# Optimization experiments

Measured on AMD Instinct MI355X. Metric: run time of the kernel, lower is better.

Reference implementation:

```python
import jax, jax.numpy as jnp
import numpy as np

N, E = 50000, 800000
IN_DIM, OUT_DIM, H = 256, 128, 8
GEO_HID = 16  # RBF feature dim and geo_mlp hidden dim


def setup_inputs() -> dict:
    key = jax.random.key(0)
    ks = jax.random.split(key, 16)
    def lin(k, fan_out, fan_in):
        kw, kb = jax.random.split(k)
        lim = 1.0 / np.sqrt(fan_in)
        W = jax.random.uniform(kw, (fan_out, fan_in), jnp.float32, -lim, lim)
        b = jax.random.uniform(kb, (fan_out,), jnp.float32, -lim, lim)
        return W, b
    Wq, bq = lin(ks[0], OUT_DIM, IN_DIM)
    Wk, bk = lin(ks[1], OUT_DIM, IN_DIM)
    Wv, bv = lin(ks[2], OUT_DIM, IN_DIM)
    Wo, bo = lin(ks[3], OUT_DIM, OUT_DIM)
    Wg1, bg1 = lin(ks[4], GEO_HID, GEO_HID)
    Wg2, bg2 = lin(ks[5], H, GEO_HID)
    x = jax.random.normal(ks[6], (N, IN_DIM), jnp.float32)
    edge_index = jax.random.randint(ks[7], (2, E), 0, N, jnp.int64)
    edge_dist = jax.random.uniform(ks[8], (E,), jnp.float32) * 6.0
    return {"x": x, "edge_index": edge_index, "edge_dist": edge_dist,
            "Wq": Wq, "bq": bq, "Wk": Wk, "bk": bk, "Wv": Wv, "bv": bv,
            "Wo": Wo, "bo": bo, "Wg1": Wg1, "bg1": bg1, "Wg2": Wg2, "bg2": bg2}


def reference(x, edge_index, edge_dist, Wq, bq, Wk, bk, Wv, bv, Wo, bo, Wg1, bg1, Wg2, bg2):
    n = x.shape[0]
    num_heads = Wg2.shape[0]
    head_dim = Wq.shape[0] // num_heads
    scale = 1.0 / (head_dim ** 0.5)

    q = (x @ Wq.T + bq).reshape(n, num_heads, head_dim)
    k = (x @ Wk.T + bk).reshape(n, num_heads, head_dim)
    v = (x @ Wv.T + bv).reshape(n, num_heads, head_dim)

    # RBF expansion: 16 centers in [0, 6], gamma = 1.0
    centers = jnp.linspace(0.0, 6.0, GEO_HID)
    rbf = jnp.exp(-(edge_dist[:, None] - centers) ** 2)          # [E, 16]
    geo_bias = jax.nn.relu(rbf @ Wg1.T + bg1) @ Wg2.T + bg2      # [E, H]

    row, col = edge_index[0], edge_index[1]
    attn = (q[row] * k[col]).sum(-1) * scale + geo_bias          # [E, H]

    # segment softmax over incoming edges per destination node (row)
    m = jax.ops.segment_max(attn, row, num_segments=n)           # [N, H]
    e = jnp.exp(attn - m[row])
    s = jax.ops.segment_sum(e, row, num_segments=n)              # [N, H]
    a = e / (s[row] + 1e-12)                                     # [E, H]

    out = jax.ops.segment_sum(v[col] * a[:, :, None], row, num_segments=n)
    out = out.reshape(n, num_heads * head_dim)
    return out @ Wo.T + bo
```

## Files before the change

### kernel.cpp

```cpp
#include <hip/hip_runtime.h>
#include <math.h>

#define IN_DIM 256
#define OUT_DIM 128
#define NH 8
#define HD 16
#define GH 16
#define TBL 1024
#define LOG2E 1.44269504f
#define RCAP 64
#define BINSH 6
#define BCAP 1408

typedef __attribute__((ext_vector_type(8))) short short8;
typedef __attribute__((ext_vector_type(4))) float floatx4;

__device__ __forceinline__ unsigned short f2bf(float f) {
    union { float f; unsigned u; } v; v.f = f;
    unsigned r = v.u + 0x7fffu + ((v.u >> 16) & 1u);
    return (unsigned short)(r >> 16);
}
__device__ __forceinline__ float bf2f(unsigned short h) {
    union { unsigned u; float f; } v; v.u = ((unsigned)h) << 16;
    return v.f;
}
__device__ __forceinline__ void split1(float f, unsigned short& h, unsigned short& l) {
    h = f2bf(f);
    l = f2bf(f - bf2f(h));
}
__device__ __forceinline__ float bflo(unsigned u) { return __uint_as_float(u << 16); }
__device__ __forceinline__ float bfhi(unsigned u) { return __uint_as_float(u & 0xffff0000u); }

__global__ __launch_bounds__(256) void prep_all_kernel(
    const float* __restrict__ Wq, const float* __restrict__ Wk,
    const float* __restrict__ Wv, const float* __restrict__ Wo,
    unsigned short* __restrict__ wh, unsigned short* __restrict__ wl,
    unsigned short* __restrict__ wo_h, unsigned short* __restrict__ wo_l,
    const float* __restrict__ Wg1, const float* __restrict__ bg1,
    const float* __restrict__ Wg2, const float* __restrict__ bg2,
    float* __restrict__ tbl, int* __restrict__ gbin,
    int nbins, int nwm, int nwo, int ngeo) {
    int bx = blockIdx.x;
    int t = threadIdx.x;

    if (bx < 3 * nwm) {
        int m = bx / nwm;
        int i = (bx - m * nwm) * 256 + t;
        if (i >= (OUT_DIM * IN_DIM) / 4) return;
        const float* W = (m == 0) ? Wq : (m == 1) ? Wk : Wv;
        float4 f = ((const float4*)W)[i];
        ushort4 h, l;
        split1(f.x, h.x, l.x); split1(f.y, h.y, l.y);
        split1(f.z, h.z, l.z); split1(f.w, h.w, l.w);
        size_t base = (size_t)m * (OUT_DIM * IN_DIM) / 4;
        ((ushort4*)wh)[base + i] = h;
        ((ushort4*)wl)[base + i] = l;
        return;
    }
    bx -= 3 * nwm;
    if (bx < nwo) {
        int i = bx * 256 + t;
        if (i >= (OUT_DIM * OUT_DIM) / 4) return;
        float4 f = ((const float4*)Wo)[i];
        ushort4 h, l;
        split1(f.x, h.x, l.x); split1(f.y, h.y, l.y);
        split1(f.z, h.z, l.z); split1(f.w, h.w, l.w);
        ((ushort4*)wo_h)[i] = h;
        ((ushort4*)wo_l)[i] = l;
        return;
    }
    bx -= nwo;
    if (bx < ngeo) {
        int i = bx * 256 + t;
        if (i >= TBL) return;
        float d = (float)i * (6.0f / (float)(TBL - 1));
        float rbf[GH];
#pragma unroll
        for (int j = 0; j < GH; ++j) {
            float c = 0.4f * (float)j;
            float tt = d - c;
            rbf[j] = __expf(-tt * tt);
        }
        float hid[GH];
#pragma unroll
        for (int j = 0; j < GH; ++j) {
            float acc = bg1[j];
#pragma unroll
            for (int kk = 0; kk < GH; ++kk) acc += rbf[kk] * Wg1[j * GH + kk];
            hid[j] = fmaxf(acc, 0.0f);
        }
#pragma unroll
        for (int h = 0; h < NH; ++h) {
            float acc = bg2[h];
#pragma unroll
            for (int j = 0; j < GH; ++j) acc += hid[j] * Wg2[h * GH + j];
            tbl[i * NH + h] = acc * LOG2E;
        }
        return;
    }
    for (int i = t; i < nbins; i += 256) gbin[i] = 0;
}

__global__ __launch_bounds__(512, 4) void qkv_kernel(
    const float* __restrict__ x,
    const unsigned short* __restrict__ wh, const unsigned short* __restrict__ wl,
    const float* __restrict__ bq, const float* __restrict__ bk, const float* __restrict__ bv,
    float* __restrict__ q, unsigned short* __restrict__ kb, unsigned short* __restrict__ vb,
    const int* __restrict__ ei, const float* __restrict__ edist,
    int* __restrict__ gbin, int2* __restrict__ binbuf,
    int Nn, int E_, int nxb, int nb1, int nbins) {
    __shared__ unsigned short xh_s[128 * 40];
    __shared__ unsigned short xl_s[128 * 40];
    __shared__ unsigned short wh_s[128 * 40];
    __shared__ unsigned short wl_s[128 * 40];

    const int tid = threadIdx.x;
    int bx = blockIdx.x;

    if (bx < nb1) {
        int* hist = (int*)xh_s;
        const int e0 = bx * 4096;
        for (int b = tid; b < nbins; b += 512) hist[b] = 0;
        __syncthreads();
#pragma unroll
        for (int i = 0; i < 8; ++i) {
            int e = e0 + tid + i * 512;
            if (e < E_) atomicAdd(&hist[ei[e] >> BINSH], 1);
        }
        __syncthreads();
        for (int b = tid; b < nbins; b += 512) {
            int h = hist[b];
            int base = 0;
            if (h) base = atomicAdd(&gbin[b], h);
            hist[b] = base;
        }
        __syncthreads();
#pragma unroll
        for (int i = 0; i < 8; ++i) {
            int e = e0 + tid + i * 512;
            if (e < E_) {
                int row = ei[e];
                int bin = row >> BINSH;
                int r = atomicAdd(&hist[bin], 1);
                float u = edist[e] * ((float)(TBL - 1) / 6.0f);
                u = fminf(fmaxf(u, 0.0f), (float)(TBL - 1));
                if (r < BCAP)
                    binbuf[(size_t)bin * BCAP + r] =
                        make_int2((ei[E_ + e] & 0x1FFFF) | ((row & 63) << 17), __float_as_int(u));
            }
        }
        return;
    }
    bx -= nb1;

    const int wsel = bx / nxb;
    const int n0 = (bx - wsel * nxb) * 128;
    const unsigned short* W_h = wh + (size_t)wsel * (OUT_DIM * IN_DIM);
    const unsigned short* W_l = wl + (size_t)wsel * (OUT_DIM * IN_DIM);
    const float* bias = (wsel == 0) ? bq : (wsel == 1) ? bk : bv;
    const bool vpath = (wsel == 2);

    const int w = tid >> 6;
    const int lane = tid & 63;
    const int ml = lane & 15;
    const int quad = lane >> 4;
    const int rg = w & 3;
    const int cg = w >> 2;

    const int rows_valid = min(128, Nn - n0);

    floatx4 acc[2][4];
#pragma unroll
    for (int rr = 0; rr < 2; ++rr)
#pragma unroll
        for (int ct = 0; ct < 4; ++ct) acc[rr][ct] = (floatx4){0.f, 0.f, 0.f, 0.f};

    const int r = tid >> 2, c = tid & 3;
    const bool rvld = (r < rows_valid);
    const float* xrow = x + (size_t)(n0 + r) * IN_DIM + c * 8;
    const unsigned short* wrow_h = W_h + (size_t)r * IN_DIM + c * 8;
    const unsigned short* wrow_l = W_l + (size_t)r * IN_DIM + c * 8;

    float4 xa = {0.f, 0.f, 0.f, 0.f}, xb = {0.f, 0.f, 0.f, 0.f};
    short8 wreg_h, wreg_l;
    if (rvld) { xa = ((const float4*)xrow)[0]; xb = ((const float4*)xrow)[1]; }
    wreg_h = *(const short8*)(wrow_h);
    if (vpath) wreg_l = *(const short8*)(wrow_l);

    for (int kci = 0; kci < 8; ++kci) {
        {
            float xf[8] = {xa.x, xa.y, xa.z, xa.w, xb.x, xb.y, xb.z, xb.w};
            if (!vpath) {
                unsigned short hv[8];
#pragma unroll
                for (int j = 0; j < 8; ++j) hv[j] = f2bf(xf[j]);
                *(short8*)(xh_s + r * 40 + c * 8) = *(short8*)hv;
                *(short8*)(wh_s + r * 40 + c * 8) = wreg_h;
            } else {
                unsigned short hv[8], lv[8];
#pragma unroll
                for (int j = 0; j < 8; ++j) split1(xf[j], hv[j], lv[j]);
                *(short8*)(xh_s + r * 40 + c * 8) = *(short8*)hv;
                *(short8*)(xl_s + r * 40 + c * 8) = *(short8*)lv;
                *(short8*)(wh_s + r * 40 + c * 8) = wreg_h;
                *(short8*)(wl_s + r * 40 + c * 8) = wreg_l;
            }
        }
        if (kci < 7) {
            const int koff = (kci + 1) * 32;
            if (rvld) {
                xa = ((const float4*)(xrow + koff))[0];
                xb = ((const float4*)(xrow + koff))[1];
            }
            wreg_h = *(const short8*)(wrow_h + koff);
            if (vpath) wreg_l = *(const short8*)(wrow_l + koff);
        }
        __syncthreads();

        short8 ah0 = *(const short8*)(xh_s + (rg * 32 + ml) * 40 + quad * 8);
        short8 ah1 = *(const short8*)(xh_s + (rg * 32 + 16 + ml) * 40 + quad * 8);
        if (!vpath) {
#pragma unroll
            for (int ct = 0; ct < 4; ++ct) {
                short8 bh = *(const short8*)(wh_s + (cg * 64 + ct * 16 + ml) * 40 + quad * 8);
                acc[0][ct] = __builtin_amdgcn_mfma_f32_16x16x32_bf16(ah0, bh, acc[0][ct], 0, 0, 0);
                acc[1][ct] = __builtin_amdgcn_mfma_f32_16x16x32_bf16(ah1, bh, acc[1][ct], 0, 0, 0);
            }
        } else {
            short8 al0 = *(const short8*)(xl_s + (rg * 32 + ml) * 40 + quad * 8);
            short8 al1 = *(const short8*)(xl_s + (rg * 32 + 16 + ml) * 40 + quad * 8);
#pragma unroll
            for (int ct = 0; ct < 4; ++ct) {
                short8 bh = *(const short8*)(wh_s + (cg * 64 + ct * 16 + ml) * 40 + quad * 8);
                short8 bl = *(const short8*)(wl_s + (cg * 64 + ct * 16 + ml) * 40 + quad * 8);
                acc[0][ct] = __builtin_amdgcn_mfma_f32_16x16x32_bf16(ah0, bh, acc[0][ct], 0, 0, 0);
                acc[0][ct] = __builtin_amdgcn_mfma_f32_16x16x32_bf16(al0, bh, acc[0][ct], 0, 0, 0);
                acc[0][ct] = __builtin_amdgcn_mfma_f32_16x16x32_bf16(ah0, bl, acc[0][ct], 0, 0, 0);
                acc[1][ct] = __builtin_amdgcn_mfma_f32_16x16x32_bf16(ah1, bh, acc[1][ct], 0, 0, 0);
                acc[1][ct] = __builtin_amdgcn_mfma_f32_16x16x32_bf16(al1, bh, acc[1][ct], 0, 0, 0);
                acc[1][ct] = __builtin_amdgcn_mfma_f32_16x16x32_bf16(ah1, bl, acc[1][ct], 0, 0, 0);
            }
        }
        __syncthreads();
    }

    if (wsel == 0) {
#pragma unroll
        for (int rr = 0; rr < 2; ++rr)
#pragma unroll
            for (int ct = 0; ct < 4; ++ct) {
                int col = cg * 64 + ct * 16 + ml;
                float bj = bias[col];
#pragma unroll
                for (int rr2 = 0; rr2 < 4; ++rr2) {
                    int grow = n0 + rg * 32 + rr * 16 + quad * 4 + rr2;
                    if (grow < Nn) q[(size_t)grow * 128 + col] = acc[rr][ct][rr2] + bj;
                }
            }
    } else {
        unsigned short* ob = (wsel == 1) ? kb : vb;
#pragma unroll
        for (int rr = 0; rr < 2; ++rr)
#pragma unroll
            for (int ct = 0; ct < 4; ++ct) {
                int col = cg * 64 + ct * 16 + ml;
                float bj = bias[col];
#pragma unroll
                for (int rr2 = 0; rr2 < 4; ++rr2) {
                    int grow = n0 + rg * 32 + rr * 16 + quad * 4 + rr2;
                    if (grow < Nn) ob[(size_t)grow * 128 + col] = f2bf(acc[rr][ct][rr2] + bj);
                }
            }
    }
}

__global__ __launch_bounds__(256) void bin2bucket_kernel(
    const int2* __restrict__ binbuf, const int* __restrict__ gbin,
    int2* __restrict__ bucket, int2* __restrict__ meta, int Nn) {
    __shared__ int rcnt[64];
    __shared__ int pref[64];
    __shared__ int2 ebuf[BCAP];
    const int bin = blockIdx.x;
    const int t = threadIdx.x;
    if (t < 64) rcnt[t] = 0;
    __syncthreads();
    int nb = gbin[bin];
    if (nb > BCAP) nb = BCAP;
    const int row0 = bin << BINSH;

    int px[6], py[6], rk[6];
#pragma unroll
    for (int j = 0; j < 6; ++j) {
        int i = t + j * 256;
        rk[j] = -1;
        if (i < nb) {
            int2 p = binbuf[(size_t)bin * BCAP + i];
            int rowrel = (p.x >> 17) & 63;
            int r = atomicAdd(&rcnt[rowrel], 1);
            if (r < RCAP) { px[j] = p.x & 0x1FFFF; py[j] = p.y; rk[j] = r | (rowrel << 16); }
        }
    }
    __syncthreads();
    int myclamp = 0;
    if (t < 64) { myclamp = min(rcnt[t], RCAP); pref[t] = myclamp; }
    __syncthreads();
    for (int off = 1; off < 64; off <<= 1) {
        int v = 0;
        if (t < 64 && t >= off) v = pref[t - off];
        __syncthreads();
        if (t < 64) pref[t] += v;
        __syncthreads();
    }
#pragma unroll
    for (int j = 0; j < 6; ++j) {
        if (rk[j] >= 0) {
            int rowrel = rk[j] >> 16;
            int r = rk[j] & 0xFFFF;
            int pos = pref[rowrel] - min(rcnt[rowrel], RCAP) + r;
            ebuf[pos] = make_int2(px[j], py[j]);
        }
    }
    __syncthreads();
    int total = pref[63];
    const int obase = bin * BCAP;
    for (int i = t; i < total; i += 256) bucket[obase + i] = ebuf[i];
    if (t < 64 && row0 + t < Nn)
        meta[row0 + t] = make_int2(obase + pref[t] - myclamp, myclamp);
}

__global__ __launch_bounds__(256) void fused_node_kernel(
    const float* __restrict__ q, const unsigned short* __restrict__ kb,
    const unsigned short* __restrict__ vb, const int2* __restrict__ bucket,
    const float* __restrict__ tbl, const int2* __restrict__ meta,
    float* __restrict__ o, int Nn) {
    const int lane = threadIdx.x & 63;
    const int g = lane >> 3;
    const int h = lane & 7;
    const int n = blockIdx.x * 4 + (threadIdx.x >> 6);
    if (n >= Nn) return;

    const int2 m = meta[n];
    const int start = m.x;
    const int c = m.y;
    const int end = start + c;

    float qf[16];
    {
        const float4* qp = (const float4*)(q + (size_t)n * 128 + h * 16);
#pragma unroll
        for (int j = 0; j < 4; ++j) {
            float4 t = qp[j];
            qf[j * 4 + 0] = t.x; qf[j * 4 + 1] = t.y;
            qf[j * 4 + 2] = t.z; qf[j * 4 + 3] = t.w;
        }
    }

    float l = 0.0f;
    float acc[16];
#pragma unroll
    for (int j = 0; j < 16; ++j) acc[j] = 0.0f;

    auto edge_math = [&](const uint4& k0, const uint4& k1, const uint4& v0, const uint4& v1,
                         float u, bool valid) {
        unsigned kk[8] = {k0.x, k0.y, k0.z, k0.w, k1.x, k1.y, k1.z, k1.w};
        float d = 0.0f;
#pragma unroll
        for (int j = 0; j < 8; ++j) {
            d = fmaf(bflo(kk[j]), qf[2 * j], d);
            d = fmaf(bfhi(kk[j]), qf[2 * j + 1], d);
        }
        int i0 = min((int)u, TBL - 2);
        float fr = u - (float)i0;
        float t0 = tbl[i0 * NH + h];
        float t1 = tbl[i0 * NH + NH + h];
        float logit2 = fmaf(d, 0.25f * LOG2E, fmaf(fr, t1 - t0, t0));
        logit2 = fminf(logit2, 80.0f);
        if (!valid) logit2 = -1e30f;
        float p = __builtin_amdgcn_exp2f(logit2);
        l += p;
        unsigned vv[8] = {v0.x, v0.y, v0.z, v0.w, v1.x, v1.y, v1.z, v1.w};
#pragma unroll
        for (int j = 0; j < 8; ++j) {
            acc[2 * j]     = fmaf(p, bflo(vv[j]), acc[2 * j]);
            acc[2 * j + 1] = fmaf(p, bfhi(vv[j]), acc[2 * j + 1]);
        }
    };

    if (c > 0) {
        int2 npA = bucket[min(start + g, end - 1)];
        const bool vAv = (start + g < end);
        const bool doB = (end > start + 8);
        int2 npB = npA;
        bool vBv = false;
        if (doB) {
            npB = bucket[min(start + 8 + g, end - 1)];
            vBv = (start + 8 + g < end);
        }
        const uint4* kpA = (const uint4*)(kb + (size_t)npA.x * 128 + h * 16);
        const uint4* vpA = (const uint4*)(vb + (size_t)npA.x * 128 + h * 16);
        uint4 kA0 = kpA[0], kA1 = kpA[1], vA0 = vpA[0], vA1 = vpA[1];
        uint4 kB0, kB1, vB0, vB1;
        if (doB) {
            const uint4* kpB = (const uint4*)(kb + (size_t)npB.x * 128 + h * 16);
            const uint4* vpB = (const uint4*)(vb + (size_t)npB.x * 128 + h * 16);
            kB0 = kpB[0]; kB1 = kpB[1]; vB0 = vpB[0]; vB1 = vpB[1];
        }
        edge_math(kA0, kA1, vA0, vA1, __int_as_float(npA.y), vAv);
        if (doB) edge_math(kB0, kB1, vB0, vB1, __int_as_float(npB.y), vBv);
        for (int base = start + 16; base < end; base += 8) {
            int2 np = bucket[min(base + g, end - 1)];
            bool valid = (base + g < end);
            const uint4* kp = (const uint4*)(kb + (size_t)np.x * 128 + h * 16);
            const uint4* vp = (const uint4*)(vb + (size_t)np.x * 128 + h * 16);
            uint4 k0 = kp[0], k1 = kp[1], v0 = vp[0], v1 = vp[1];
            edge_math(k0, k1, v0, v1, __int_as_float(np.y), valid);
        }
    }

#pragma unroll
    for (int off = 8; off < 64; off <<= 1) {
        l += __shfl_xor(l, off);
#pragma unroll
        for (int j = 0; j < 16; ++j) acc[j] += __shfl_xor(acc[j], off);
    }

    if (g == 0) {
        float inv = 1.0f / (l + 1e-12f);
        float4* op = (float4*)(o + (size_t)n * 128 + h * 16);
#pragma unroll
        for (int j = 0; j < 4; ++j) {
            float4 t;
            t.x = acc[j * 4 + 0] * inv; t.y = acc[j * 4 + 1] * inv;
            t.z = acc[j * 4 + 2] * inv; t.w = acc[j * 4 + 3] * inv;
            op[j] = t;
        }
    }
}

__global__ __launch_bounds__(512, 4) void out_gemm_mfma_kernel(
    const float* __restrict__ o,
    const unsigned short* __restrict__ wo_h, const unsigned short* __restrict__ wo_l,
    const float* __restrict__ bo, float* __restrict__ out, int Nn) {
    const int n0 = blockIdx.x * 128;

    __shared__ unsigned short xh_s[128 * 40];
    __shared__ unsigned short xl_s[128 * 40];
    __shared__ unsigned short wh_s[128 * 40];
    __shared__ unsigned short wl_s[128 * 40];

    const int tid = threadIdx.x;
    const int w = tid >> 6;
    const int lane = tid & 63;
    const int ml = lane & 15;
    const int quad = lane >> 4;
    const int rg = w & 3;
    const int cg = w >> 2;

    const int rows_valid = min(128, Nn - n0);

    floatx4 acc[2][4];
#pragma unroll
    for (int rr = 0; rr < 2; ++rr)
#pragma unroll
        for (int ct = 0; ct < 4; ++ct) acc[rr][ct] = (floatx4){0.f, 0.f, 0.f, 0.f};

    const int r = tid >> 2, c = tid & 3;
    const bool rvld = (r < rows_valid);
    const float* orow = o + (size_t)(n0 + r) * OUT_DIM + c * 8;
    const unsigned short* wrow_h = wo_h + (size_t)r * OUT_DIM + c * 8;
    const unsigned short* wrow_l = wo_l + (size_t)r * OUT_DIM + c * 8;

    float4 oa = {0.f, 0.f, 0.f, 0.f}, ob2 = {0.f, 0.f, 0.f, 0.f};
    short8 wreg_h, wreg_l;
    if (rvld) { oa = ((const float4*)orow)[0]; ob2 = ((const float4*)orow)[1]; }
    wreg_h = *(const short8*)(wrow_h);
    wreg_l = *(const short8*)(wrow_l);

    for (int kci = 0; kci < 4; ++kci) {
        {
            float xf[8] = {oa.x, oa.y, oa.z, oa.w, ob2.x, ob2.y, ob2.z, ob2.w};
            unsigned short hv[8], lv[8];
#pragma unroll
            for (int j = 0; j < 8; ++j) split1(xf[j], hv[j], lv[j]);
            *(short8*)(xh_s + r * 40 + c * 8) = *(short8*)hv;
            *(short8*)(xl_s + r * 40 + c * 8) = *(short8*)lv;
            *(short8*)(wh_s + r * 40 + c * 8) = wreg_h;
            *(short8*)(wl_s + r * 40 + c * 8) = wreg_l;
        }
        if (kci < 3) {
            const int koff = (kci + 1) * 32;
            if (rvld) {
                oa  = ((const float4*)(orow + koff))[0];
                ob2 = ((const float4*)(orow + koff))[1];
            }
            wreg_h = *(const short8*)(wrow_h + koff);
            wreg_l = *(const short8*)(wrow_l + koff);
        }
        __syncthreads();

        short8 ah0 = *(const short8*)(xh_s + (rg * 32 + ml) * 40 + quad * 8);
        short8 ah1 = *(const short8*)(xh_s + (rg * 32 + 16 + ml) * 40 + quad * 8);
        short8 al0 = *(const short8*)(xl_s + (rg * 32 + ml) * 40 + quad * 8);
        short8 al1 = *(const short8*)(xl_s + (rg * 32 + 16 + ml) * 40 + quad * 8);
#pragma unroll
        for (int ct = 0; ct < 4; ++ct) {
            short8 bh = *(const short8*)(wh_s + (cg * 64 + ct * 16 + ml) * 40 + quad * 8);
            short8 bl = *(const short8*)(wl_s + (cg * 64 + ct * 16 + ml) * 40 + quad * 8);
            acc[0][ct] = __builtin_amdgcn_mfma_f32_16x16x32_bf16(ah0, bh, acc[0][ct], 0, 0, 0);
            acc[0][ct] = __builtin_amdgcn_mfma_f32_16x16x32_bf16(al0, bh, acc[0][ct], 0, 0, 0);
            acc[0][ct] = __builtin_amdgcn_mfma_f32_16x16x32_bf16(ah0, bl, acc[0][ct], 0, 0, 0);
            acc[1][ct] = __builtin_amdgcn_mfma_f32_16x16x32_bf16(ah1, bh, acc[1][ct], 0, 0, 0);
            acc[1][ct] = __builtin_amdgcn_mfma_f32_16x16x32_bf16(al1, bh, acc[1][ct], 0, 0, 0);
            acc[1][ct] = __builtin_amdgcn_mfma_f32_16x16x32_bf16(ah1, bl, acc[1][ct], 0, 0, 0);
        }
        __syncthreads();
    }

#pragma unroll
    for (int rr = 0; rr < 2; ++rr)
#pragma unroll
        for (int ct = 0; ct < 4; ++ct) {
            int col = cg * 64 + ct * 16 + ml;
            float bj = bo[col];
#pragma unroll
            for (int rr2 = 0; rr2 < 4; ++rr2) {
                int grow = n0 + rg * 32 + rr * 16 + quad * 4 + rr2;
                if (grow < Nn) out[(size_t)grow * 128 + col] = acc[rr][ct][rr2] + bj;
            }
        }
}

extern "C" void kernel_launch(void* const* d_in, const int* in_sizes, int n_in,
                              void* d_out, int out_size, void* d_ws, size_t ws_size,
                              hipStream_t stream) {
    const float* x   = (const float*)d_in[0];
    const int* ei    = (const int*)d_in[1];
    const float* edist = (const float*)d_in[2];
    const float* Wq = (const float*)d_in[3];  const float* bq = (const float*)d_in[4];
    const float* Wk = (const float*)d_in[5];  const float* bk = (const float*)d_in[6];
    const float* Wv = (const float*)d_in[7];  const float* bv = (const float*)d_in[8];
    const float* Wo = (const float*)d_in[9];  const float* bo = (const float*)d_in[10];
    const float* Wg1 = (const float*)d_in[11]; const float* bg1 = (const float*)d_in[12];
    const float* Wg2 = (const float*)d_in[13]; const float* bg2 = (const float*)d_in[14];
    const int Nn = in_sizes[0] / IN_DIM;
    const int Ee = in_sizes[2];
    float* out = (float*)d_out;

    char* ws = (char*)d_ws;
    size_t off = 0;
    auto alloc = [&](size_t bytes) -> char* {
        char* p = ws + off;
        off += (bytes + 255) & ~(size_t)255;
        return p;
    };
    float* q  = (float*)alloc((size_t)Nn * 128 * 4);
    unsigned short* kbuf = (unsigned short*)alloc((size_t)Nn * 128 * 2);
    unsigned short* vbuf = (unsigned short*)alloc((size_t)Nn * 128 * 2);
    float* o = (float*)alloc((size_t)Nn * 128 * 4);
    float* geot = (float*)alloc((size_t)TBL * 8 * 4);
    int2* meta = (int2*)alloc((size_t)Nn * 8);
    int nbins = (Nn + 63) >> BINSH;
    int* gbin = (int*)alloc((size_t)nbins * 4);
    unsigned short* wh_all = (unsigned short*)alloc((size_t)3 * OUT_DIM * IN_DIM * 2);
    unsigned short* wl_all = (unsigned short*)alloc((size_t)3 * OUT_DIM * IN_DIM * 2);
    unsigned short* wo_h = (unsigned short*)alloc((size_t)OUT_DIM * OUT_DIM * 2);
    unsigned short* wo_l = (unsigned short*)alloc((size_t)OUT_DIM * OUT_DIM * 2);
    int2* bucket = (int2*)alloc((size_t)nbins * BCAP * 8);

    int2* binbuf = (int2*)o;

    int nwm = ((OUT_DIM * IN_DIM / 4) + 255) / 256;
    int nwo = ((OUT_DIM * OUT_DIM / 4) + 255) / 256;
    int ngeo = (TBL + 255) / 256;
    int gprep = 3 * nwm + nwo + ngeo + 1;
    prep_all_kernel<<<gprep, 256, 0, stream>>>(
        Wq, Wk, Wv, Wo, wh_all, wl_all, wo_h, wo_l,
        Wg1, bg1, Wg2, bg2, geot, gbin, nbins, nwm, nwo, ngeo);

    int nxb = (Nn + 127) / 128;
    int nb1 = (Ee + 4095) / 4096;
    qkv_kernel<<<nb1 + 3 * nxb, 512, 0, stream>>>(
        x, wh_all, wl_all, bq, bk, bv, q, kbuf, vbuf,
        ei, edist, gbin, binbuf, Nn, Ee, nxb, nb1, nbins);

    bin2bucket_kernel<<<nbins, 256, 0, stream>>>(binbuf, gbin, bucket, meta, Nn);

    fused_node_kernel<<<(Nn + 3) / 4, 256, 0, stream>>>(q, kbuf, vbuf, bucket, geot, meta, o, Nn);

    out_gemm_mfma_kernel<<<(Nn + 127) / 128, 512, 0, stream>>>(o, wo_h, wo_l, bo, out, Nn);
}
```

Measured before the change: 256.0 us.

## Load MFMA operands directly from global memory, dropping LDS staging and barriers

The QKV and output-projection GEMM kernels no longer stage x and W tiles through shared memory. Each lane now loads its MFMA fragments straight from global memory, with the bf16 split done in registers, and all per-iteration __syncthreads are removed. The aim is to cut LDS traffic, barrier stalls and shared-memory footprint, which may allow higher occupancy. In exchange, each x row is read by two wave column-groups and each weight row by four row-groups, so redundant global/L2 loads increase and the explicit register prefetch pipelining is lost.

```diff
diff --git a/kernel.cpp b/kernel.cpp
--- a/kernel.cpp
+++ b/kernel.cpp
@@ -109,30 +109,26 @@
     const int* __restrict__ ei, const float* __restrict__ edist,
     int* __restrict__ gbin, int2* __restrict__ binbuf,
     int Nn, int E_, int nxb, int nb1, int nbins) {
-    __shared__ unsigned short xh_s[128 * 40];
-    __shared__ unsigned short xl_s[128 * 40];
-    __shared__ unsigned short wh_s[128 * 40];
-    __shared__ unsigned short wl_s[128 * 40];
+    __shared__ int hist_s[1024];
 
     const int tid = threadIdx.x;
     int bx = blockIdx.x;
 
     if (bx < nb1) {
-        int* hist = (int*)xh_s;
         const int e0 = bx * 4096;
-        for (int b = tid; b < nbins; b += 512) hist[b] = 0;
+        for (int b = tid; b < nbins; b += 512) hist_s[b] = 0;
         __syncthreads();
 #pragma unroll
         for (int i = 0; i < 8; ++i) {
             int e = e0 + tid + i * 512;
-            if (e < E_) atomicAdd(&hist[ei[e] >> BINSH], 1);
+            if (e < E_) atomicAdd(&hist_s[ei[e] >> BINSH], 1);
         }
         __syncthreads();
         for (int b = tid; b < nbins; b += 512) {
-            int h = hist[b];
+            int h = hist_s[b];
             int base = 0;
             if (h) base = atomicAdd(&gbin[b], h);
-            hist[b] = base;
+            hist_s[b] = base;
         }
         __syncthreads();
 #pragma unroll
@@ -141,7 +137,7 @@
             if (e < E_) {
                 int row = ei[e];
                 int bin = row >> BINSH;
-                int r = atomicAdd(&hist[bin], 1);
+                int r = atomicAdd(&hist_s[bin], 1);
                 float u = edist[e] * ((float)(TBL - 1) / 6.0f);
                 u = fminf(fmaxf(u, 0.0f), (float)(TBL - 1));
                 if (r < BCAP)
@@ -167,7 +163,21 @@
     const int rg = w & 3;
     const int cg = w >> 2;
 
-    const int rows_valid = min(128, Nn - n0);
+    const int r0 = n0 + rg * 32 + ml;
+    const int r1 = r0 + 16;
+    const bool v0r = (r0 < Nn);
+    const bool v1r = (r1 < Nn);
+    const float* xr0 = x + (size_t)r0 * IN_DIM + quad * 8;
+    const float* xr1 = x + (size_t)r1 * IN_DIM + quad * 8;
+
+    const unsigned short* wph[4];
+    const unsigned short* wpl[4];
+#pragma unroll
+    for (int ct = 0; ct < 4; ++ct) {
+        int col = cg * 64 + ct * 16 + ml;
+        wph[ct] = W_h + (size_t)col * IN_DIM + quad * 8;
+        wpl[ct] = W_l + (size_t)col * IN_DIM + quad * 8;
+    }
 
     floatx4 acc[2][4];
 #pragma unroll
@@ -175,64 +185,47 @@
 #pragma unroll
         for (int ct = 0; ct < 4; ++ct) acc[rr][ct] = (floatx4){0.f, 0.f, 0.f, 0.f};
 
-    const int r = tid >> 2, c = tid & 3;
-    const bool rvld = (r < rows_valid);
-    const float* xrow = x + (size_t)(n0 + r) * IN_DIM + c * 8;
-    const unsigned short* wrow_h = W_h + (size_t)r * IN_DIM + c * 8;
-    const unsigned short* wrow_l = W_l + (size_t)r * IN_DIM + c * 8;
-
-    float4 xa = {0.f, 0.f, 0.f, 0.f}, xb = {0.f, 0.f, 0.f, 0.f};
-    short8 wreg_h, wreg_l;
-    if (rvld) { xa = ((const float4*)xrow)[0]; xb = ((const float4*)xrow)[1]; }
-    wreg_h = *(const short8*)(wrow_h);
-    if (vpath) wreg_l = *(const short8*)(wrow_l);
-
+#pragma unroll 2
     for (int kci = 0; kci < 8; ++kci) {
-        {
-            float xf[8] = {xa.x, xa.y, xa.z, xa.w, xb.x, xb.y, xb.z, xb.w};
-            if (!vpath) {
-                unsigned short hv[8];
-#pragma unroll
-                for (int j = 0; j < 8; ++j) hv[j] = f2bf(xf[j]);
-                *(short8*)(xh_s + r * 40 + c * 8) = *(short8*)hv;
-                *(short8*)(wh_s + r * 40 + c * 8) = wreg_h;
-            } else {
-                unsigned short hv[8], lv[8];
-#pragma unroll
-                for (int j = 0; j < 8; ++j) split1(xf[j], hv[j], lv[j]);
-                *(short8*)(xh_s + r * 40 + c * 8) = *(short8*)hv;
-                *(short8*)(xl_s + r * 40 + c * 8) = *(short8*)lv;
-                *(short8*)(wh_s + r * 40 + c * 8) = wreg_h;
-                *(short8*)(wl_s + r * 40 + c * 8) = wreg_l;
-            }
-        }
-        if (kci < 7) {
-            const int koff = (kci + 1) * 32;
-            if (rvld) {
-                xa = ((const float4*)(xrow + koff))[0];
-                xb = ((const float4*)(xrow + koff))[1];
-            }
-            wreg_h = *(const short8*)(wrow_h + koff);
-            if (vpath) wreg_l = *(const short8*)(wrow_l + koff);
-        }
-        __syncthreads();
-
-        short8 ah0 = *(const short8*)(xh_s + (rg * 32 + ml) * 40 + quad * 8);
-        short8 ah1 = *(const short8*)(xh_s + (rg * 32 + 16 + ml) * 40 + quad * 8);
+        const int koff = kci * 32;
+        float a0[8] = {0.f,0.f,0.f,0.f,0.f,0.f,0.f,0.f};
+        float a1[8] = {0.f,0.f,0.f,0.f,0.f,0.f,0.f,0.f};
+        if (v0r) {
+            float4 t0 = ((const float4*)(xr0 + koff))[0];
+            float4 t1 = ((const float4*)(xr0 + koff))[1];
+            a0[0]=t0.x; a0[1]=t0.y; a0[2]=t0.z; a0[3]=t0.w;
+            a0[4]=t1.x; a0[5]=t1.y; a0[6]=t1.z; a0[7]=t1.w;
+        }
+        if (v1r) {
+            float4 t0 = ((const float4*)(xr1 + koff))[0];
+            float4 t1 = ((const float4*)(xr1 + koff))[1];
+            a1[0]=t0.x; a1[1]=t0.y; a1[2]=t0.z; a1[3]=t0.w;
+            a1[4]=t1.x; a1[5]=t1.y; a1[6]=t1.z; a1[7]=t1.w;
+        }
         if (!vpath) {
+            unsigned short h0[8], h1[8];
+#pragma unroll
+            for (int j = 0; j < 8; ++j) { h0[j] = f2bf(a0[j]); h1[j] = f2bf(a1[j]); }
+            short8 ah0 = *(short8*)h0;
+            short8 ah1 = *(short8*)h1;
 #pragma unroll
             for (int ct = 0; ct < 4; ++ct) {
-                short8 bh = *(const short8*)(wh_s + (cg * 64 + ct * 16 + ml) * 40 + quad * 8);
+                short8 bh = *(const short8*)(wph[ct] + koff);
                 acc[0][ct] = __builtin_amdgcn_mfma_f32_16x16x32_bf16(ah0, bh, acc[0][ct], 0, 0, 0);
                 acc[1][ct] = __builtin_amdgcn_mfma_f32_16x16x32_bf16(ah1, bh, acc[1][ct], 0, 0, 0);
             }
         } else {
-            short8 al0 = *(const short8*)(xl_s + (rg * 32 + ml) * 40 + quad * 8);
-            short8 al1 = *(const short8*)(xl_s + (rg * 32 + 16 + ml) * 40 + quad * 8);
+            unsigned short h0[8], l0[8], h1[8], l1[8];
+#pragma unroll
+            for (int j = 0; j < 8; ++j) { split1(a0[j], h0[j], l0[j]); split1(a1[j], h1[j], l1[j]); }
+            short8 ah0 = *(short8*)h0;
+            short8 al0 = *(short8*)l0;
+            short8 ah1 = *(short8*)h1;
+            short8 al1 = *(short8*)l1;
 #pragma unroll
             for (int ct = 0; ct < 4; ++ct) {
-                short8 bh = *(const short8*)(wh_s + (cg * 64 + ct * 16 + ml) * 40 + quad * 8);
-                short8 bl = *(const short8*)(wl_s + (cg * 64 + ct * 16 + ml) * 40 + quad * 8);
+                short8 bh = *(const short8*)(wph[ct] + koff);
+                short8 bl = *(const short8*)(wpl[ct] + koff);
                 acc[0][ct] = __builtin_amdgcn_mfma_f32_16x16x32_bf16(ah0, bh, acc[0][ct], 0, 0, 0);
                 acc[0][ct] = __builtin_amdgcn_mfma_f32_16x16x32_bf16(al0, bh, acc[0][ct], 0, 0, 0);
                 acc[0][ct] = __builtin_amdgcn_mfma_f32_16x16x32_bf16(ah0, bl, acc[0][ct], 0, 0, 0);
@@ -241,7 +234,6 @@
                 acc[1][ct] = __builtin_amdgcn_mfma_f32_16x16x32_bf16(ah1, bl, acc[1][ct], 0, 0, 0);
             }
         }
-        __syncthreads();
     }
 
     if (wsel == 0) {
@@ -443,11 +435,6 @@
     const float* __restrict__ bo, float* __restrict__ out, int Nn) {
     const int n0 = blockIdx.x * 128;
 
-    __shared__ unsigned short xh_s[128 * 40];
-    __shared__ unsigned short xl_s[128 * 40];
-    __shared__ unsigned short wh_s[128 * 40];
-    __shared__ unsigned short wl_s[128 * 40];
-
     const int tid = threadIdx.x;
     const int w = tid >> 6;
     const int lane = tid & 63;
@@ -456,7 +443,21 @@
     const int rg = w & 3;
     const int cg = w >> 2;
 
-    const int rows_valid = min(128, Nn - n0);
+    const int r0 = n0 + rg * 32 + ml;
+    const int r1 = r0 + 16;
+    const bool v0r = (r0 < Nn);
+    const bool v1r = (r1 < Nn);
+    const float* or0 = o + (size_t)r0 * OUT_DIM + quad * 8;
+    const float* or1 = o + (size_t)r1 * OUT_DIM + quad * 8;
+
+    const unsigned short* wph[4];
+    const unsigned short* wpl[4];
+#pragma unroll
+    for (int ct = 0; ct < 4; ++ct) {
+        int col = cg * 64 + ct * 16 + ml;
+        wph[ct] = wo_h + (size_t)col * OUT_DIM + quad * 8;
+        wpl[ct] = wo_l + (size_t)col * OUT_DIM + quad * 8;
+    }
 
     floatx4 acc[2][4];
 #pragma unroll
@@ -464,48 +465,34 @@
 #pragma unroll
         for (int ct = 0; ct < 4; ++ct) acc[rr][ct] = (floatx4){0.f, 0.f, 0.f, 0.f};
 
-    const int r = tid >> 2, c = tid & 3;
-    const bool rvld = (r < rows_valid);
-    const float* orow = o + (size_t)(n0 + r) * OUT_DIM + c * 8;
-    const unsigned short* wrow_h = wo_h + (size_t)r * OUT_DIM + c * 8;
-    const unsigned short* wrow_l = wo_l + (size_t)r * OUT_DIM + c * 8;
-
-    float4 oa = {0.f, 0.f, 0.f, 0.f}, ob2 = {0.f, 0.f, 0.f, 0.f};
-    short8 wreg_h, wreg_l;
-    if (rvld) { oa = ((const float4*)orow)[0]; ob2 = ((const float4*)orow)[1]; }
-    wreg_h = *(const short8*)(wrow_h);
-    wreg_l = *(const short8*)(wrow_l);
-
+#pragma unroll 2
     for (int kci = 0; kci < 4; ++kci) {
-        {
-            float xf[8] = {oa.x, oa.y, oa.z, oa.w, ob2.x, ob2.y, ob2.z, ob2.w};
-            unsigned short hv[8], lv[8];
-#pragma unroll
-            for (int j = 0; j < 8; ++j) split1(xf[j], hv[j], lv[j]);
-            *(short8*)(xh_s + r * 40 + c * 8) = *(short8*)hv;
-            *(short8*)(xl_s + r * 40 + c * 8) = *(short8*)lv;
-            *(short8*)(wh_s + r * 40 + c * 8) = wreg_h;
-            *(short8*)(wl_s + r * 40 + c * 8) = wreg_l;
-        }
-        if (kci < 3) {
-            const int koff = (kci + 1) * 32;
-            if (rvld) {
-                oa  = ((const float4*)(orow + koff))[0];
-                ob2 = ((const float4*)(orow + koff))[1];
-            }
-            wreg_h = *(const short8*)(wrow_h + koff);
-            wreg_l = *(const short8*)(wrow_l + koff);
-        }
-        __syncthreads();
-
-        short8 ah0 = *(const short8*)(xh_s + (rg * 32 + ml) * 40 + quad * 8);
-        short8 ah1 = *(const short8*)(xh_s + (rg * 32 + 16 + ml) * 40 + quad * 8);
-        short8 al0 = *(const short8*)(xl_s + (rg * 32 + ml) * 40 + quad * 8);
-        short8 al1 = *(const short8*)(xl_s + (rg * 32 + 16 + ml) * 40 + quad * 8);
+        const int koff = kci * 32;
+        float a0[8] = {0.f,0.f,0.f,0.f,0.f,0.f,0.f,0.f};
+        float a1[8] = {0.f,0.f,0.f,0.f,0.f,0.f,0.f,0.f};
+        if (v0r) {
+            float4 t0 = ((const float4*)(or0 + koff))[0];
+            float4 t1 = ((const float4*)(or0 + koff))[1];
+            a0[0]=t0.x; a0[1]=t0.y; a0[2]=t0.z; a0[3]=t0.w;
+            a0[4]=t1.x; a0[5]=t1.y; a0[6]=t1.z; a0[7]=t1.w;
+        }
+        if (v1r) {
+            float4 t0 = ((const float4*)(or1 + koff))[0];
+            float4 t1 = ((const float4*)(or1 + koff))[1];
+            a1[0]=t0.x; a1[1]=t0.y; a1[2]=t0.z; a1[3]=t0.w;
+            a1[4]=t1.x; a1[5]=t1.y; a1[6]=t1.z; a1[7]=t1.w;
+        }
+        unsigned short h0[8], l0[8], h1[8], l1[8];
+#pragma unroll
+        for (int j = 0; j < 8; ++j) { split1(a0[j], h0[j], l0[j]); split1(a1[j], h1[j], l1[j]); }
+        short8 ah0 = *(short8*)h0;
+        short8 al0 = *(short8*)l0;
+        short8 ah1 = *(short8*)h1;
+        short8 al1 = *(short8*)l1;
 #pragma unroll
         for (int ct = 0; ct < 4; ++ct) {
-            short8 bh = *(const short8*)(wh_s + (cg * 64 + ct * 16 + ml) * 40 + quad * 8);
-            short8 bl = *(const short8*)(wl_s + (cg * 64 + ct * 16 + ml) * 40 + quad * 8);
+            short8 bh = *(const short8*)(wph[ct] + koff);
+            short8 bl = *(const short8*)(wpl[ct] + koff);
             acc[0][ct] = __builtin_amdgcn_mfma_f32_16x16x32_bf16(ah0, bh, acc[0][ct], 0, 0, 0);
             acc[0][ct] = __builtin_amdgcn_mfma_f32_16x16x32_bf16(al0, bh, acc[0][ct], 0, 0, 0);
             acc[0][ct] = __builtin_amdgcn_mfma_f32_16x16x32_bf16(ah0, bl, acc[0][ct], 0, 0, 0);
@@ -513,7 +500,6 @@
             acc[1][ct] = __builtin_amdgcn_mfma_f32_16x16x32_bf16(al1, bh, acc[1][ct], 0, 0, 0);
             acc[1][ct] = __builtin_amdgcn_mfma_f32_16x16x32_bf16(ah1, bl, acc[1][ct], 0, 0, 0);
         }
-        __syncthreads();
     }
 
 #pragma unroll
```

Measured after the change: 330.8 us. +29.2%, slower.
